# Kernel tuning notes

Measured on AMD Instinct MI355X. Metric: run time of the kernel, lower is better.

## Reference

```python
import jax, jax.numpy as jnp
import numpy as np

N_BCH = 8        # molecules per batch
N_ATM = 10000    # atoms per molecule
N_EDGE = 5_120_000  # ~avg degree 64
N_ELM = 100      # element-type table size


def setup_inputs() -> dict:
    key = jax.random.key(0)
    k1, k2, k3, k4, k5, k6, k7 = jax.random.split(key, 7)
    elm = jax.random.randint(k1, (N_BCH, N_ATM), 0, N_ELM)
    edge_n = jax.random.randint(k2, (N_EDGE,), 0, N_BCH)
    edge_i = jax.random.randint(k3, (N_EDGE,), 0, N_ATM)
    edge_j = jax.random.randint(k4, (N_EDGE,), 0, N_ATM)
    # squared distances in [0, 4) -> dis in [0, 2)
    sod = jax.random.uniform(k5, (N_EDGE,), dtype=jnp.float32) * 4.0
    # per-element force constant and radius (positive)
    k_param = jax.random.uniform(k6, (N_ELM,), dtype=jnp.float32) + 0.5
    radius = jax.random.uniform(k7, (N_ELM,), dtype=jnp.float32) * 0.5 + 0.5
    return {"elm": elm, "edge_n": edge_n, "edge_i": edge_i, "edge_j": edge_j,
            "sod": sod, "k": k_param, "radius": radius}


def reference(elm, edge_n, edge_i, edge_j, sod, k, radius):
    # gather per-edge element types
    ei = elm[edge_n, edge_i]          # [E]
    ej = elm[edge_n, edge_j]          # [E]
    dis = jnp.sqrt(sod)               # [E]
    kk = k[ei] + k[ej]                # [E]
    R = radius[ei] + radius[ej]       # [E]
    mask = dis < R
    d = dis - R
    eng_bnd = jnp.where(mask, kk * d * d, jnp.zeros((), dtype=sod.dtype))  # [E]
    # scatter-add per atom: flat index n*n_atm + i
    seg = edge_n * N_ATM + edge_i
    eng_atm = jax.ops.segment_sum(eng_bnd, seg, num_segments=N_BCH * N_ATM)
    eng_atm = eng_atm.reshape(N_BCH, N_ATM)
    eng_mol = eng_atm.sum(axis=1)     # [n_bch]
    return eng_mol
```

## Files before the change

### kernel.cpp

```cpp
#include <hip/hip_runtime.h>
#include <hip/hip_bf16.h>
#include <hip/hip_fp16.h>

#define N_BCH 8
#define N_ATM 10000
#define N_ELM 100
#define N_ATOMS_TOT (N_BCH * N_ATM)

typedef int   i4 __attribute__((ext_vector_type(4)));
typedef float f4 __attribute__((ext_vector_type(4)));

__launch_bounds__(256)
__global__ void pack_elm_kernel(const int* __restrict__ elm,
                                unsigned int* __restrict__ elm_u8_as_u32,
                                float* __restrict__ out) {
    int t = blockIdx.x * blockDim.x + threadIdx.x;
    if (t < N_ATOMS_TOT / 4) {
        i4 v = *(const i4*)(elm + 4 * t);
        unsigned int packed = (unsigned int)(v[0] & 0xff)
                            | ((unsigned int)(v[1] & 0xff) << 8)
                            | ((unsigned int)(v[2] & 0xff) << 16)
                            | ((unsigned int)(v[3] & 0xff) << 24);
        elm_u8_as_u32[t] = packed;
    }
    if (blockIdx.x == 0 && threadIdx.x < N_BCH) out[threadIdx.x] = 0.0f;
}

__launch_bounds__(1024, 8)
__global__ void edge_kernel(const unsigned int* __restrict__ elm_u8,
                            const float* __restrict__ kparam,
                            const float* __restrict__ radius,
                            const int* __restrict__ edge_n,
                            const int* __restrict__ edge_i,
                            const int* __restrict__ edge_j,
                            const float* __restrict__ sod,
                            float* __restrict__ out,
                            int nE) {
    __shared__ unsigned int s_elm32[N_ATOMS_TOT / 4];
    __shared__ __half2 s_kr[128];
    __shared__ float s_red[16][N_BCH];

    {
        const i4* src = (const i4*)elm_u8;
        i4* dst = (i4*)s_elm32;
        for (int t = threadIdx.x; t < N_ATOMS_TOT / 16; t += 1024)
            dst[t] = src[t];
        if (threadIdx.x < N_ELM)
            s_kr[threadIdx.x] =
                __floats2half2_rn(kparam[threadIdx.x], radius[threadIdx.x]);
    }
    __syncthreads();

    const unsigned char* s_elm = (const unsigned char*)s_elm32;

    float acc[N_BCH];
#pragma unroll
    for (int b = 0; b < N_BCH; ++b) acc[b] = 0.0f;

    const int tid    = blockIdx.x * blockDim.x + threadIdx.x;
    const int stride = gridDim.x * blockDim.x;
    const int nvec   = nE >> 2;

    const i4* en4 = (const i4*)edge_n;
    const i4* ei4 = (const i4*)edge_i;
    const i4* ej4 = (const i4*)edge_j;
    const f4* s4  = (const f4*)sod;

    for (int v = tid; v < nvec; v += stride) {
        i4 nn = __builtin_nontemporal_load(en4 + v);
        i4 ii = __builtin_nontemporal_load(ei4 + v);
        i4 jj = __builtin_nontemporal_load(ej4 + v);
        f4 ss = __builtin_nontemporal_load(s4  + v);

#pragma unroll
        for (int u = 0; u < 4; ++u) {
            int n = nn[u];
            int base = n * N_ATM;
            int e_i = s_elm[base + ii[u]];
            int e_j = s_elm[base + jj[u]];
            __half2 krsum = __hadd2(s_kr[e_i], s_kr[e_j]);
            float kk = __low2float(krsum);
            float R  = __high2float(krsum);
            float dis = sqrtf(ss[u]);
            float d  = dis - R;
            float val = (dis < R) ? kk * d * d : 0.0f;
#pragma unroll
            for (int b = 0; b < N_BCH; ++b)
                acc[b] += (n == b) ? val : 0.0f;
        }
    }

    const int tail_start = nvec << 2;
    const int tail_n = nE - tail_start;
    if (tid < tail_n) {
        int e = tail_start + tid;
        int n = edge_n[e];
        int e_i = s_elm[n * N_ATM + edge_i[e]];
        int e_j = s_elm[n * N_ATM + edge_j[e]];
        __half2 krsum = __hadd2(s_kr[e_i], s_kr[e_j]);
        float kk = __low2float(krsum);
        float R  = __high2float(krsum);
        float dis = sqrtf(sod[e]);
        float d  = dis - R;
        float val = (dis < R) ? kk * d * d : 0.0f;
#pragma unroll
        for (int b = 0; b < N_BCH; ++b)
            acc[b] += (n == b) ? val : 0.0f;
    }

    const int lane = threadIdx.x & 63;
    const int wave = threadIdx.x >> 6;

#pragma unroll
    for (int off = 8; off <= 32; off <<= 1) {
#pragma unroll
        for (int b = 0; b < N_BCH; ++b)
            acc[b] += __shfl_xor(acc[b], off, 64);
    }
    const int j = lane >> 3;
    float x = acc[0];
#pragma unroll
    for (int b = 1; b < N_BCH; ++b) x = (j == b) ? acc[b] : x;
#pragma unroll
    for (int off = 1; off <= 4; off <<= 1)
        x += __shfl_xor(x, off, 64);

    if ((lane & 7) == 0) s_red[wave][j] = x;
    __syncthreads();
    if (threadIdx.x < N_BCH) {
        float v = 0.0f;
#pragma unroll
        for (int w = 0; w < 16; ++w) v += s_red[w][threadIdx.x];
        atomicAdd(&out[threadIdx.x], v);
    }
}

extern "C" void kernel_launch(void* const* d_in, const int* in_sizes, int n_in,
                              void* d_out, int out_size, void* d_ws, size_t ws_size,
                              hipStream_t stream) {
    const int*   elm    = (const int*)d_in[0];
    const int*   edge_n = (const int*)d_in[1];
    const int*   edge_i = (const int*)d_in[2];
    const int*   edge_j = (const int*)d_in[3];
    const float* sod    = (const float*)d_in[4];
    const float* kparam = (const float*)d_in[5];
    const float* radius = (const float*)d_in[6];
    float* out = (float*)d_out;
    const int nE = in_sizes[1];

    unsigned int* elm_u8 = (unsigned int*)d_ws;

    hipLaunchKernelGGL(pack_elm_kernel, dim3((N_ATOMS_TOT / 4 + 255) / 256),
                       dim3(256), 0, stream, elm, elm_u8, out);
    hipLaunchKernelGGL(edge_kernel, dim3(512), dim3(1024), 0, stream,
                       elm_u8, kparam, radius, edge_n, edge_i, edge_j, sod,
                       out, nE);
}
```

Baseline: 126.2 us.

## Fuse elm packing into edge kernel, use contiguous block chunks with register prefetch

Removes the separate pack kernel: each block now reads the int32 element table and packs it to bytes in shared memory itself, and the output is zeroed with a memset. The grid shrinks to 256 blocks, each handling a contiguous chunk of edges, and the next iteration's vector loads are issued before the current iteration's compute to overlap memory latency. Every block now reads the full int elm array (four times the bytes of the packed table), so redundant global reads increase. Fewer blocks may reduce occupancy.

Measured after the change: 130.0 us. +3.1%, slower.

```diff
diff --git a/kernel.cpp b/kernel.cpp
--- a/kernel.cpp
+++ b/kernel.cpp
@@ -5,29 +5,15 @@
 #define N_BCH 8
 #define N_ATM 10000
 #define N_ELM 100
-#define N_ATOMS_TOT (N_BCH * N_ATM)
+#define N_ATOMS_TOT 80000
+#define NBLK 256
+#define NTHR 1024
 
 typedef int   i4 __attribute__((ext_vector_type(4)));
 typedef float f4 __attribute__((ext_vector_type(4)));
 
-__launch_bounds__(256)
-__global__ void pack_elm_kernel(const int* __restrict__ elm,
-                                unsigned int* __restrict__ elm_u8_as_u32,
-                                float* __restrict__ out) {
-    int t = blockIdx.x * blockDim.x + threadIdx.x;
-    if (t < N_ATOMS_TOT / 4) {
-        i4 v = *(const i4*)(elm + 4 * t);
-        unsigned int packed = (unsigned int)(v[0] & 0xff)
-                            | ((unsigned int)(v[1] & 0xff) << 8)
-                            | ((unsigned int)(v[2] & 0xff) << 16)
-                            | ((unsigned int)(v[3] & 0xff) << 24);
-        elm_u8_as_u32[t] = packed;
-    }
-    if (blockIdx.x == 0 && threadIdx.x < N_BCH) out[threadIdx.x] = 0.0f;
-}
-
-__launch_bounds__(1024, 8)
-__global__ void edge_kernel(const unsigned int* __restrict__ elm_u8,
+__launch_bounds__(1024, 4)
+__global__ void edge_kernel(const int* __restrict__ elm,
                             const float* __restrict__ kparam,
                             const float* __restrict__ radius,
                             const int* __restrict__ edge_n,
@@ -40,15 +26,16 @@
     __shared__ __half2 s_kr[128];
     __shared__ float s_red[16][N_BCH];
 
-    {
-        const i4* src = (const i4*)elm_u8;
-        i4* dst = (i4*)s_elm32;
-        for (int t = threadIdx.x; t < N_ATOMS_TOT / 16; t += 1024)
-            dst[t] = src[t];
-        if (threadIdx.x < N_ELM)
-            s_kr[threadIdx.x] =
-                __floats2half2_rn(kparam[threadIdx.x], radius[threadIdx.x]);
+    for (int t = threadIdx.x; t < N_ATOMS_TOT / 4; t += NTHR) {
+        i4 v = *(const i4*)(elm + 4 * t);
+        s_elm32[t] = (unsigned int)(v[0] & 0xff)
+                   | ((unsigned int)(v[1] & 0xff) << 8)
+                   | ((unsigned int)(v[2] & 0xff) << 16)
+                   | ((unsigned int)(v[3] & 0xff) << 24);
     }
+    if (threadIdx.x < N_ELM)
+        s_kr[threadIdx.x] =
+            __floats2half2_rn(kparam[threadIdx.x], radius[threadIdx.x]);
     __syncthreads();
 
     const unsigned char* s_elm = (const unsigned char*)s_elm32;
@@ -57,43 +44,58 @@
 #pragma unroll
     for (int b = 0; b < N_BCH; ++b) acc[b] = 0.0f;
 
-    const int tid    = blockIdx.x * blockDim.x + threadIdx.x;
-    const int stride = gridDim.x * blockDim.x;
-    const int nvec   = nE >> 2;
+    const int nvec  = nE >> 2;
+    const int chunk = (nvec + NBLK - 1) / NBLK;
+    const int base  = blockIdx.x * chunk;
+    const int vmax  = min(base + chunk, nvec);
+    const int nsweep = (chunk + NTHR - 1) / NTHR;
 
     const i4* en4 = (const i4*)edge_n;
     const i4* ei4 = (const i4*)edge_i;
     const i4* ej4 = (const i4*)edge_j;
     const f4* s4  = (const f4*)sod;
 
-    for (int v = tid; v < nvec; v += stride) {
-        i4 nn = __builtin_nontemporal_load(en4 + v);
-        i4 ii = __builtin_nontemporal_load(ei4 + v);
-        i4 jj = __builtin_nontemporal_load(ej4 + v);
-        f4 ss = __builtin_nontemporal_load(s4  + v);
+    int  v  = base + threadIdx.x;
+    bool pv = v < vmax;
+    int  vc = pv ? v : 0;
+    i4 nn = __builtin_nontemporal_load(en4 + vc);
+    i4 ii = __builtin_nontemporal_load(ei4 + vc);
+    i4 jj = __builtin_nontemporal_load(ej4 + vc);
+    f4 ss = __builtin_nontemporal_load(s4  + vc);
+
+    for (int s = 0; s < nsweep; ++s) {
+        int  v2  = v + NTHR;
+        bool pv2 = v2 < vmax;
+        int  vc2 = pv2 ? v2 : 0;
+        i4 nn2 = __builtin_nontemporal_load(en4 + vc2);
+        i4 ii2 = __builtin_nontemporal_load(ei4 + vc2);
+        i4 jj2 = __builtin_nontemporal_load(ej4 + vc2);
+        f4 ss2 = __builtin_nontemporal_load(s4  + vc2);
 
 #pragma unroll
         for (int u = 0; u < 4; ++u) {
             int n = nn[u];
-            int base = n * N_ATM;
-            int e_i = s_elm[base + ii[u]];
-            int e_j = s_elm[base + jj[u]];
+            int bb = n * N_ATM;
+            int e_i = s_elm[bb + ii[u]];
+            int e_j = s_elm[bb + jj[u]];
             __half2 krsum = __hadd2(s_kr[e_i], s_kr[e_j]);
             float kk = __low2float(krsum);
             float R  = __high2float(krsum);
             float dis = sqrtf(ss[u]);
             float d  = dis - R;
-            float val = (dis < R) ? kk * d * d : 0.0f;
+            float val = (pv && (dis < R)) ? kk * d * d : 0.0f;
 #pragma unroll
             for (int b = 0; b < N_BCH; ++b)
                 acc[b] += (n == b) ? val : 0.0f;
         }
+        nn = nn2; ii = ii2; jj = jj2; ss = ss2; v = v2; pv = pv2;
     }
 
     const int tail_start = nvec << 2;
     const int tail_n = nE - tail_start;
-    if (tid < tail_n) {
-        int e = tail_start + tid;
+    const int gtid = blockIdx.x * NTHR + threadIdx.x;
+    if (gtid < tail_n) {
+        int e = tail_start + gtid;
         int n = edge_n[e];
         int e_i = s_elm[n * N_ATM + edge_i[e]];
         int e_j = s_elm[n * N_ATM + edge_j[e]];
@@ -110,7 +112,6 @@
 
     const int lane = threadIdx.x & 63;
     const int wave = threadIdx.x >> 6;
-
 #pragma unroll
     for (int off = 8; off <= 32; off <<= 1) {
 #pragma unroll
@@ -128,10 +129,10 @@
     if ((lane & 7) == 0) s_red[wave][j] = x;
     __syncthreads();
     if (threadIdx.x < N_BCH) {
-        float v = 0.0f;
+        float t = 0.0f;
 #pragma unroll
-        for (int w = 0; w < 16; ++w) v += s_red[w][threadIdx.x];
-        atomicAdd(&out[threadIdx.x], v);
+        for (int w = 0; w < 16; ++w) t += s_red[w][threadIdx.x];
+        atomicAdd(&out[threadIdx.x], t);
     }
 }
 
@@ -148,11 +149,9 @@
     float* out = (float*)d_out;
     const int nE = in_sizes[1];
 
-    unsigned int* elm_u8 = (unsigned int*)d_ws;
+    hipMemsetAsync(out, 0, out_size * sizeof(float), stream);
 
-    hipLaunchKernelGGL(pack_elm_kernel, dim3((N_ATOMS_TOT / 4 + 255) / 256),
-                       dim3(256), 0, stream, elm, elm_u8, out);
-    hipLaunchKernelGGL(edge_kernel, dim3(512), dim3(1024), 0, stream,
-                       elm_u8, kparam, radius, edge_n, edge_i, edge_j, sod,
+    hipLaunchKernelGGL(edge_kernel, dim3(NBLK), dim3(NTHR), 0, stream,
+                       elm, kparam, radius, edge_n, edge_i, edge_j, sod,
                        out, nE);
 }
```
